# Kernel optimization log

Hardware: AMD Instinct MI355X
Metric: run time of the kernel (lower is better)

Reference implementation:

```python
import jax, jax.numpy as jnp
from jax import lax
import numpy as np

B, N, G, K = 4, 1024, 128, 32
D_MODEL, DEPTH, CLS = 384, 12, 40
D_INNER, D_STATE, D_CONV, DT_RANK = 768, 16, 4, 24
EPS = 1e-5
BN_SCALE = 1.0 / float(np.sqrt(1.0 + EPS))  # eval BN, running_mean=0, running_var=1


def layernorm(x, w, b):
    mu = x.mean(-1, keepdims=True)
    var = ((x - mu) ** 2).mean(-1, keepdims=True)
    return (x - mu) * lax.rsqrt(var + EPS) * w + b


def bn_eval(x, g, b):
    return x * (g * BN_SCALE) + b


def fps(xyz, n):
    Bb, Nn, _ = xyz.shape
    first = jnp.zeros((Bb,), jnp.int32)

    def step(carry, _):
        dmin, last = carry
        p = jnp.take_along_axis(xyz, last[:, None, None], axis=1)  # B,1,3
        dmin = jnp.minimum(dmin, jnp.sum((xyz - p) ** 2, -1))
        nxt = jnp.argmax(dmin, -1).astype(jnp.int32)
        return (dmin, nxt), nxt

    _, rest = lax.scan(step, (jnp.full((Bb, Nn), 1e10, xyz.dtype), first), None, length=n - 1)
    return jnp.concatenate([first[None, :], rest], 0).T  # B,G


def group_points(xyz):
    idx = fps(xyz, G)
    center = jnp.take_along_axis(xyz, idx[:, :, None], axis=1)            # B,G,3
    d2 = jnp.sum((center[:, :, None, :] - xyz[:, None, :, :]) ** 2, -1)   # B,G,N
    _, knn = lax.top_k(-d2, K)                                            # B,G,K
    nb = jax.vmap(lambda p, i: p[i])(xyz, knn)                            # B,G,K,3
    return nb - center[:, :, None, :], center


def encoder(pg, w1, b1, g1, bb1, w2, b2, w3, b3, g2, bb2, w4, b4):
    Bb, Gg, Kk, _ = pg.shape
    f = pg.reshape(Bb * Gg, Kk, 3)
    f = jax.nn.relu(bn_eval(f @ w1.T + b1, g1, bb1))                      # BG,K,128
    f = f @ w2.T + b2                                                     # BG,K,256
    fg = f.max(1, keepdims=True)
    f = jnp.concatenate([jnp.broadcast_to(fg, f.shape), f], -1)           # BG,K,512
    f = jax.nn.relu(bn_eval(f @ w3.T + b3, g2, bb2))
    f = f @ w4.T + b4
    return f.max(1).reshape(Bb, Gg, -1)                                   # B,G,C


def mamba_mixer(x, ipw, cw, cb, xpw, dpw, dpb, A_log, Dp, opw):
    L = x.shape[1]
    xz = x @ ipw.T                                                        # B,L,2*Di
    u, z = jnp.split(xz, 2, -1)
    up = jnp.pad(u, ((0, 0), (D_CONV - 1, 0), (0, 0)))                    # causal depthwise conv
    u = sum(up[:, k:k + L, :] * cw[:, k] for k in range(D_CONV)) + cb
    u = jax.nn.silu(u)
    xdb = u @ xpw.T
    dt, Bm, Cm = jnp.split(xdb, [DT_RANK, DT_RANK + D_STATE], -1)
    dt = jax.nn.softplus(dt @ dpw.T + dpb)                                # B,L,Di
    A = -jnp.exp(A_log)                                                   # Di,Ds

    def step(h, inp):
        dt_t, B_t, C_t, u_t = inp
        h = jnp.exp(dt_t[:, :, None] * A) * h + (dt_t * u_t)[:, :, None] * B_t[:, None, :]
        return h, jnp.einsum('bds,bs->bd', h, C_t)

    h0 = jnp.zeros((x.shape[0], D_INNER, D_STATE), x.dtype)
    _, ys = lax.scan(step, h0, (dt.swapaxes(0, 1), Bm.swapaxes(0, 1), Cm.swapaxes(0, 1), u.swapaxes(0, 1)))
    y = ys.swapaxes(0, 1) + u * Dp
    return (y * jax.nn.silu(z)) @ opw.T


def forward(pts, enc_w1, enc_b1, enc_bn1_g, enc_bn1_b, enc_w2, enc_b2, enc_w3, enc_b3,
            enc_bn2_g, enc_bn2_b, enc_w4, enc_b4, pos_w1, pos_b1, pos_w2, pos_b2,
            ln_w, ln_b, in_proj_w, conv_w, conv_b, x_proj_w, dt_proj_w, dt_proj_b,
            A_log, D_param, out_proj_w, normf_w, normf_b, norm_w, norm_b,
            head_w1, head_b1, head_bn1_g, head_bn1_b, head_w2, head_b2,
            head_bn2_g, head_bn2_b, head_w3, head_b3):
    nb, center = group_points(pts)
    tok = encoder(nb, enc_w1, enc_b1, enc_bn1_g, enc_bn1_b, enc_w2, enc_b2,
                  enc_w3, enc_b3, enc_bn2_g, enc_bn2_b, enc_w4, enc_b4)    # B,G,384
    pos = jax.nn.gelu(center @ pos_w1.T + pos_b1, approximate=False) @ pos_w2.T + pos_b2

    # PointMamba token reordering: sort by center x, y, z and concatenate -> L = 3G
    toks, poss = [], []
    for ax in range(3):
        o = jnp.argsort(center[:, :, ax], axis=-1)[:, :, None]
        toks.append(jnp.take_along_axis(tok, o, axis=1))
        poss.append(jnp.take_along_axis(pos, o, axis=1))
    tok = jnp.concatenate(toks, 1)
    pos = jnp.concatenate(poss, 1)

    h = tok + pos
    res = jnp.zeros_like(h)

    def layer_step(carry, p):
        h, res = carry
        lnw, lnb, ipw, cw, cb, xpw, dpw, dpb, Al, Dp, opw = p
        res = h + res
        x = layernorm(res, lnw, lnb)
        h = mamba_mixer(x, ipw, cw, cb, xpw, dpw, dpb, Al, Dp, opw)
        return (h, res), None

    (h, res), _ = lax.scan(layer_step, (h, res),
                           (ln_w, ln_b, in_proj_w, conv_w, conv_b, x_proj_w,
                            dt_proj_w, dt_proj_b, A_log, D_param, out_proj_w))
    x = layernorm(h + res, normf_w, normf_b)   # MixerModel.norm_f
    x = layernorm(x, norm_w, norm_b)           # PointMamba.norm
    feat = x.mean(1)                           # B,384
    h1 = jax.nn.relu(bn_eval(feat @ head_w1.T + head_b1, head_bn1_g, head_bn1_b))
    h2 = jax.nn.relu(bn_eval(h1 @ head_w2.T + head_b2, head_bn2_g, head_bn2_b))
    return h2 @ head_w3.T + head_b3            # B,CLS


def setup_inputs():
    key = jax.random.key(0)
    ks = iter(jax.random.split(key, 64))

    def rn(shape, s=0.02):
        return jax.random.normal(next(ks), shape, jnp.float32) * s

    inp = dict(
        pts=jax.random.normal(next(ks), (B, N, 3), jnp.float32),
        enc_w1=rn((128, 3), 0.1), enc_b1=jnp.zeros((128,)),
        enc_bn1_g=jnp.ones((128,)), enc_bn1_b=jnp.zeros((128,)),
        enc_w2=rn((256, 128), 0.05), enc_b2=jnp.zeros((256,)),
        enc_w3=rn((512, 512), 0.05), enc_b3=jnp.zeros((512,)),
        enc_bn2_g=jnp.ones((512,)), enc_bn2_b=jnp.zeros((512,)),
        enc_w4=rn((D_MODEL, 512), 0.05), enc_b4=jnp.zeros((D_MODEL,)),
        pos_w1=rn((128, 3), 0.1), pos_b1=jnp.zeros((128,)),
        pos_w2=rn((D_MODEL, 128), 0.05), pos_b2=jnp.zeros((D_MODEL,)),
        ln_w=jnp.ones((DEPTH, D_MODEL)), ln_b=jnp.zeros((DEPTH, D_MODEL)),
        in_proj_w=rn((DEPTH, 2 * D_INNER, D_MODEL)),
        conv_w=rn((DEPTH, D_INNER, D_CONV), 0.2), conv_b=jnp.zeros((DEPTH, D_INNER)),
        x_proj_w=rn((DEPTH, DT_RANK + 2 * D_STATE, D_INNER)),
        dt_proj_w=rn((DEPTH, D_INNER, DT_RANK), 0.1),
        dt_proj_b=jnp.full((DEPTH, D_INNER), -4.6, jnp.float32),
        A_log=jnp.broadcast_to(jnp.log(jnp.arange(1, D_STATE + 1, dtype=jnp.float32)),
                               (DEPTH, D_INNER, D_STATE)).copy(),
        D_param=jnp.ones((DEPTH, D_INNER)),
        out_proj_w=rn((DEPTH, D_MODEL, D_INNER)),
        normf_w=jnp.ones((D_MODEL,)), normf_b=jnp.zeros((D_MODEL,)),
        norm_w=jnp.ones((D_MODEL,)), norm_b=jnp.zeros((D_MODEL,)),
        head_w1=rn((256, D_MODEL), 0.05), head_b1=jnp.zeros((256,)),
        head_bn1_g=jnp.ones((256,)), head_bn1_b=jnp.zeros((256,)),
        head_w2=rn((256, 256), 0.05), head_b2=jnp.zeros((256,)),
        head_bn2_g=jnp.ones((256,)), head_bn2_b=jnp.zeros((256,)),
        head_w3=rn((CLS, 256), 0.05), head_b3=jnp.zeros((CLS,)),
    )
    return inp


def reference(pts, enc_w1, enc_b1, enc_bn1_g, enc_bn1_b, enc_w2, enc_b2, enc_w3, enc_b3,
              enc_bn2_g, enc_bn2_b, enc_w4, enc_b4, pos_w1, pos_b1, pos_w2, pos_b2,
              ln_w, ln_b, in_proj_w, conv_w, conv_b, x_proj_w, dt_proj_w, dt_proj_b,
              A_log, D_param, out_proj_w, normf_w, normf_b, norm_w, norm_b,
              head_w1, head_b1, head_bn1_g, head_bn1_b, head_w2, head_b2,
              head_bn2_g, head_bn2_b, head_w3, head_b3):
    return forward(pts, enc_w1, enc_b1, enc_bn1_g, enc_bn1_b, enc_w2, enc_b2, enc_w3, enc_b3,
                   enc_bn2_g, enc_bn2_b, enc_w4, enc_b4, pos_w1, pos_b1, pos_w2, pos_b2,
                   ln_w, ln_b, in_proj_w, conv_w, conv_b, x_proj_w, dt_proj_w, dt_proj_b,
                   A_log, D_param, out_proj_w, normf_w, normf_b, norm_w, norm_b,
                   head_w1, head_b1, head_bn1_g, head_bn1_b, head_w2, head_b2,
                   head_bn2_g, head_bn2_b, head_w3, head_b3)
```

## Files before the change

### kernel.cpp

```cpp
#include <hip/hip_runtime.h>
#include <hip/hip_bf16.h>

using bf16 = __hip_bfloat16;
using short8  = __attribute__((ext_vector_type(8))) short;
using floatx4 = __attribute__((ext_vector_type(4))) float;
using ull = unsigned long long;

constexpr int Bn = 4, Np = 1024, Gn = 128, Kn = 32;
constexpr int DM = 384, DEPTH = 12, CLSn = 40;
constexpr int DI = 768, DSt = 16, DTR = 24;
constexpr int Ln = 384;
constexpr int NCH = 12, CHS = 32;
constexpr int XDBS = 1536*56;
constexpr float EPSf = 1e-5f;
constexpr float BNS = 0.99999500003749968752f;
constexpr float LOG2E = 1.4426950408889634f;

static __device__ __forceinline__ short f2bf(float f){
  bf16 h = __float2bfloat16(f);
  return *reinterpret_cast<short*>(&h);
}
static __device__ __forceinline__ float fsig(float x){ return 1.f/(1.f + __expf(-x)); }
static __device__ __forceinline__ float fsoftplus(float x){
  return fmaxf(x, 0.f) + __logf(1.f + __expf(-fabsf(x)));
}

template<int CTRL>
static __device__ __forceinline__ int dppmov(int x){
  return __builtin_amdgcn_update_dpp(0, x, CTRL, 0xF, 0xF, true);
}
static __device__ __forceinline__ ull redmax64(ull key){
  #define RSTEP(CTRL) { \
    int hi = (int)(unsigned)(key >> 32), lo = (int)(unsigned)key; \
    int h2 = dppmov<CTRL>(hi), l2 = dppmov<CTRL>(lo); \
    ull k2 = ((ull)(unsigned)h2 << 32) | (unsigned)l2; \
    if (k2 > key) key = k2; }
  RSTEP(0x111) RSTEP(0x112) RSTEP(0x114) RSTEP(0x118) RSTEP(0x142) RSTEP(0x143)
  #undef RSTEP
  return key;
}

__global__ __launch_bounds__(256) void fps_kernel(const float* __restrict__ pts,
                                                  float* __restrict__ center){
  int b = blockIdx.x, t = threadIdx.x;
  int w = t >> 6, lane = t & 63;
  __shared__ float xs[1024], ys[1024], zs[1024];
  __shared__ ull red[2][4];
  const float* p = pts + (size_t)b * Np * 3;
  float X[4], Y[4], Z[4], D[4];
  #pragma unroll
  for (int i = 0; i < 4; ++i){
    int n = t + 256*i;
    float a = p[n*3+0], c = p[n*3+1], e = p[n*3+2];
    X[i] = a; Y[i] = c; Z[i] = e;
    xs[n] = a; ys[n] = c; zs[n] = e;
    D[i] = 1e10f;
  }
  __syncthreads();
  float px = xs[0], py = ys[0], pz = zs[0];
  if (t == 0){
    center[(size_t)(b*Gn)*3+0] = px;
    center[(size_t)(b*Gn)*3+1] = py;
    center[(size_t)(b*Gn)*3+2] = pz;
  }
  for (int it = 1; it < Gn; ++it){
    float v = -1.f; int nbest = t;
    #pragma unroll
    for (int i = 0; i < 4; ++i){
      float dx = __fsub_rn(X[i], px);
      float dy = __fsub_rn(Y[i], py);
      float dz = __fsub_rn(Z[i], pz);
      float d  = __fadd_rn(__fadd_rn(__fmul_rn(dx,dx), __fmul_rn(dy,dy)), __fmul_rn(dz,dz));
      float dm = fminf(D[i], d); D[i] = dm;
      if (dm > v){ v = dm; nbest = t + 256*i; }
    }
    ull key = ((ull)__float_as_uint(v) << 32) | (unsigned)(Np-1 - nbest);
    key = redmax64(key);
    if (lane == 63) red[it & 1][w] = key;
    __syncthreads();
    ull k = red[it & 1][0];
    #pragma unroll
    for (int j = 1; j < 4; ++j){ ull kj = red[it & 1][j]; if (kj > k) k = kj; }
    int wn = Np-1 - (int)(unsigned)(k & 0xFFFFFFFFu);
    wn = min(max(wn, 0), Np-1);
    px = xs[wn]; py = ys[wn]; pz = zs[wn];
    if (t == 0){
      center[(size_t)(b*Gn+it)*3+0] = px;
      center[(size_t)(b*Gn+it)*3+1] = py;
      center[(size_t)(b*Gn+it)*3+2] = pz;
    }
  }
}

__global__ __launch_bounds__(256) void knn_kernel(const float* __restrict__ pts,
                                                  const float* __restrict__ center,
                                                  float* __restrict__ nb){
  int gid = blockIdx.x; int b = gid >> 7;
  __shared__ float d2[1024];
  __shared__ float rv[4]; __shared__ int ri[4];
  int t = threadIdx.x;
  float cx = center[(size_t)gid*3+0], cy = center[(size_t)gid*3+1], cz = center[(size_t)gid*3+2];
  const float* p = pts + (size_t)b * Np * 3;
  for (int n = t; n < Np; n += 256){
    float dx = __fsub_rn(cx, p[n*3+0]);
    float dy = __fsub_rn(cy, p[n*3+1]);
    float dz = __fsub_rn(cz, p[n*3+2]);
    d2[n] = __fadd_rn(__fadd_rn(__fmul_rn(dx,dx), __fmul_rn(dy,dy)), __fmul_rn(dz,dz));
  }
  __syncthreads();
  for (int kk = 0; kk < Kn; ++kk){
    float v = 3e38f; int idx = 0;
    for (int n = t; n < Np; n += 256){
      float d = d2[n];
      if (d < v || (d == v && n < idx)){ v = d; idx = n; }
    }
    ull key = ((ull)(unsigned)(~__float_as_uint(v)) << 32) | (unsigned)(Np-1 - idx);
    key = redmax64(key);
    if ((t & 63) == 63){
      rv[t>>6] = __uint_as_float(~(unsigned)(key >> 32));
      ri[t>>6] = Np-1 - (int)(unsigned)(key & 0xFFFFFFFFu);
    }
    __syncthreads();
    if (t == 0){
      float bv = rv[0]; int bi = ri[0];
      for (int w = 1; w < 4; ++w){
        if (rv[w] < bv || (rv[w] == bv && ri[w] < bi)){ bv = rv[w]; bi = ri[w]; }
      }
      bi = min(max(bi, 0), Np-1);
      nb[((size_t)gid*Kn+kk)*3+0] = __fsub_rn(p[bi*3+0], cx);
      nb[((size_t)gid*Kn+kk)*3+1] = __fsub_rn(p[bi*3+1], cy);
      nb[((size_t)gid*Kn+kk)*3+2] = __fsub_rn(p[bi*3+2], cz);
      d2[bi] = 3e38f;
    }
    __syncthreads();
  }
}

__global__ __launch_bounds__(256) void cvt_all(const float* __restrict__ s0,
    const float* __restrict__ s1, const float* __restrict__ s2,
    const float* __restrict__ s3, const float* __restrict__ s4,
    const float* __restrict__ s5, bf16* __restrict__ dst){
  long i = ((long)blockIdx.x*256 + threadIdx.x)*4;
  if (i >= 11624448L) return;
  const float* s; long off;
  if      (i <  7077888L){ s = s0; off = 0L; }
  else if (i < 10616832L){ s = s1; off =  7077888L; }
  else if (i < 11132928L){ s = s2; off = 10616832L; }
  else if (i < 11165696L){ s = s3; off = 11132928L; }
  else if (i < 11427840L){ s = s4; off = 11165696L; }
  else                   { s = s5; off = 11427840L; }
  float4 v = *(const float4*)(s + (i - off));
  short* o = (short*)dst + i;
  o[0] = f2bf(v.x); o[1] = f2bf(v.y); o[2] = f2bf(v.z); o[3] = f2bf(v.w);
}

template<typename AT, typename WT, int ACT, int MODE, typename CT = float>
__global__ __launch_bounds__(256) void gemm_mfma(const AT* __restrict__ A, int lda,
                                                 const WT* __restrict__ W,
                                                 const float* __restrict__ bias,
                                                 const float* __restrict__ gz,
                                                 const float* __restrict__ bbp,
                                                 CT* __restrict__ C, int ldc,
                                                 int M, int N, int K){
  __shared__ __align__(16) short As[64*40];
  __shared__ __align__(16) short Ws[64*40];
  int bm = blockIdx.x * 64, bn = blockIdx.y * 64;
  int t = threadIdx.x;
  int row = t >> 2;
  int kseg = (t & 3) * 8;
  int w = t >> 6, lane = t & 63, m16 = lane & 15, q = lane >> 4;
  floatx4 acc[4] = {};
  for (int k0 = 0; k0 < K; k0 += 32){
    {
      const float* Ar = (const float*)A + (size_t)(bm + row)*lda;
      short* dst = &As[row*40 + kseg];
      #pragma unroll
      for (int j = 0; j < 8; ++j){
        int k = k0 + kseg + j;
        dst[j] = (k < K) ? f2bf(Ar[k]) : (short)0;
      }
    }
    {
      int n = bn + row;
      short* dst = &Ws[row*40 + kseg];
      #pragma unroll
      for (int j = 0; j < 8; ++j){
        int k = k0 + kseg + j;
        dst[j] = (n < N && k < K) ? f2bf(((const float*)W)[(size_t)n*K + k]) : (short)0;
      }
    }
    __syncthreads();
    short8 af = *(const short8*)&As[(w*16 + m16)*40 + q*8];
    #pragma unroll
    for (int j = 0; j < 4; ++j){
      short8 bfr = *(const short8*)&Ws[(j*16 + m16)*40 + q*8];
      acc[j] = __builtin_amdgcn_mfma_f32_16x16x32_bf16(af, bfr, acc[j], 0, 0, 0);
    }
    __syncthreads();
  }
  #pragma unroll
  for (int j = 0; j < 4; ++j){
    int n = bn + j*16 + m16;
    if (n < N){
      float bv = bias ? bias[n] : 0.f;
      float gv = 0.f, bbv = 0.f;
      if (ACT == 1){ gv = gz[n] * BNS; bbv = bbp[n]; }
      #pragma unroll
      for (int r = 0; r < 4; ++r){
        int m = bm + w*16 + q*4 + r;
        float v = acc[j][r] + bv;
        if (ACT == 1){ v = v * gv + bbv; v = fmaxf(v, 0.f); }
        if constexpr (sizeof(CT) == 2) C[(size_t)m*ldc + n] = __float2bfloat16(v);
        else                           C[(size_t)m*ldc + n] = v;
      }
    }
  }
}

template<typename AT, typename WT, int ACT, int MODE, typename CT = float>
__global__ __launch_bounds__(256) void gemm_mfma64(const AT* __restrict__ A, int lda,
                                                   const WT* __restrict__ W,
                                                   const float* __restrict__ bias,
                                                   const float* __restrict__ gz,
                                                   const float* __restrict__ bbp,
                                                   CT* __restrict__ C, int ldc,
                                                   int M, int N, int K){
  __shared__ __align__(16) short As[64*72];
  __shared__ __align__(16) short Ws[64*72];
  int bm = blockIdx.x * 64, bn = blockIdx.y * 64;
  int t = threadIdx.x;
  int row = t >> 2;
  int kseg = (t & 3) * 16;
  int w = t >> 6, lane = t & 63, m16 = lane & 15, q = lane >> 4;
  floatx4 acc[4] = {};
  for (int k0 = 0; k0 < K; k0 += 64){
    if constexpr (MODE == 1){
      const float* Yr = (const float*)A + (size_t)(bm + row)*lda + k0 + kseg;
      const float* Zr = gz + (size_t)(bm + row)*1536 + 768 + k0 + kseg;
      float y[16], z[16];
      #pragma unroll
      for (int j = 0; j < 4; ++j){
        *(float4*)&y[j*4] = *(const float4*)(Yr + j*4);
        *(float4*)&z[j*4] = *(const float4*)(Zr + j*4);
      }
      short* dst = &As[row*72 + kseg];
      #pragma unroll
      for (int jj = 0; jj < 16; ++jj) dst[jj] = f2bf(y[jj] * (z[jj] * fsig(z[jj])));
    } else if constexpr (sizeof(AT) == 2){
      const short* Ar = (const short*)A + (size_t)(bm + row)*lda + k0 + kseg;
      *(short8*)&As[row*72 + kseg]     = *(const short8*)Ar;
      *(short8*)&As[row*72 + kseg + 8] = *(const short8*)(Ar + 8);
    } else {
      const float* Ar = (const float*)A + (size_t)(bm + row)*lda + k0 + kseg;
      float a[16];
      #pragma unroll
      for (int j = 0; j < 4; ++j) *(float4*)&a[j*4] = *(const float4*)(Ar + j*4);
      short* dst = &As[row*72 + kseg];
      #pragma unroll
      for (int jj = 0; jj < 16; ++jj) dst[jj] = f2bf(a[jj]);
    }
    {
      int n = bn + row;
      if constexpr (sizeof(WT) == 2){
        short8 v0, v1;
        #pragma unroll
        for (int j = 0; j < 8; ++j){ v0[j] = 0; v1[j] = 0; }
        if (n < N){
          const short* Wr = (const short*)W + (size_t)n*K + k0 + kseg;
          v0 = *(const short8*)Wr;
          v1 = *(const short8*)(Wr + 8);
        }
        *(short8*)&Ws[row*72 + kseg]     = v0;
        *(short8*)&Ws[row*72 + kseg + 8] = v1;
      } else {
        short* dst = &Ws[row*72 + kseg];
        if (n < N){
          const float* Wr = (const float*)W + (size_t)n*K + k0 + kseg;
          float wv[16];
          #pragma unroll
          for (int j = 0; j < 4; ++j) *(float4*)&wv[j*4] = *(const float4*)(Wr + j*4);
          #pragma unroll
          for (int jj = 0; jj < 16; ++jj) dst[jj] = f2bf(wv[jj]);
        } else {
          #pragma unroll
          for (int jj = 0; jj < 16; ++jj) dst[jj] = 0;
        }
      }
    }
    __syncthreads();
    short8 af0 = *(const short8*)&As[(w*16 + m16)*72 + q*8];
    short8 af1 = *(const short8*)&As[(w*16 + m16)*72 + 32 + q*8];
    #pragma unroll
    for (int j = 0; j < 4; ++j){
      short8 b0 = *(const short8*)&Ws[(j*16 + m16)*72 + q*8];
      acc[j] = __builtin_amdgcn_mfma_f32_16x16x32_bf16(af0, b0, acc[j], 0, 0, 0);
      short8 b1 = *(const short8*)&Ws[(j*16 + m16)*72 + 32 + q*8];
      acc[j] = __builtin_amdgcn_mfma_f32_16x16x32_bf16(af1, b1, acc[j], 0, 0, 0);
    }
    __syncthreads();
  }
  #pragma unroll
  for (int j = 0; j < 4; ++j){
    int n = bn + j*16 + m16;
    if (n < N){
      float bv = bias ? bias[n] : 0.f;
      float gv = 0.f, bbv = 0.f;
      if (ACT == 1){ gv = gz[n] * BNS; bbv = bbp[n]; }
      #pragma unroll
      for (int r = 0; r < 4; ++r){
        int m = bm + w*16 + q*4 + r;
        float v = acc[j][r] + bv;
        if (ACT == 1){ v = v * gv + bbv; v = fmaxf(v, 0.f); }
        if constexpr (sizeof(CT) == 2) C[(size_t)m*ldc + n] = __float2bfloat16(v);
        else                           C[(size_t)m*ldc + n] = v;
      }
    }
  }
}

template<typename AT, typename WT, int ACT, typename CT = float>
__global__ __launch_bounds__(256) void gemm_mfma128(const AT* __restrict__ A, int lda,
                                                    const WT* __restrict__ W,
                                                    const float* __restrict__ bias,
                                                    const float* __restrict__ gz,
                                                    const float* __restrict__ bbp,
                                                    CT* __restrict__ C, int ldc,
                                                    int M, int N, int K){
  __shared__ __align__(16) short As[64*72];
  __shared__ __align__(16) short Ws[128*72];
  int bm = blockIdx.x * 64, bn = blockIdx.y * 128;
  int t = threadIdx.x;
  int row = t >> 2;
  int kseg = (t & 3) * 16;
  int row2 = t >> 1;
  int kseg2 = (t & 1) * 32;
  int w = t >> 6, lane = t & 63, m16 = lane & 15, q = lane >> 4;
  floatx4 acc[8] = {};
  for (int k0 = 0; k0 < K; k0 += 64){
    if constexpr (sizeof(AT) == 2){
      const short* Ar = (const short*)A + (size_t)(bm + row)*lda + k0 + kseg;
      *(short8*)&As[row*72 + kseg]     = *(const short8*)Ar;
      *(short8*)&As[row*72 + kseg + 8] = *(const short8*)(Ar + 8);
    } else {
      const float* Ar = (const float*)A + (size_t)(bm + row)*lda + k0 + kseg;
      float a[16];
      #pragma unroll
      for (int j = 0; j < 4; ++j) *(float4*)&a[j*4] = *(const float4*)(Ar + j*4);
      short* dst = &As[row*72 + kseg];
      #pragma unroll
      for (int jj = 0; jj < 16; ++jj) dst[jj] = f2bf(a[jj]);
    }
    {
      int n = bn + row2;
      if constexpr (sizeof(WT) == 2){
        short8 v0, v1, v2, v3;
        #pragma unroll
        for (int j = 0; j < 8; ++j){ v0[j] = 0; v1[j] = 0; v2[j] = 0; v3[j] = 0; }
        if (n < N){
          const short* Wr = (const short*)W + (size_t)n*K + k0 + kseg2;
          v0 = *(const short8*)Wr;
          v1 = *(const short8*)(Wr + 8);
          v2 = *(const short8*)(Wr + 16);
          v3 = *(const short8*)(Wr + 24);
        }
        *(short8*)&Ws[row2*72 + kseg2]      = v0;
        *(short8*)&Ws[row2*72 + kseg2 + 8]  = v1;
        *(short8*)&Ws[row2*72 + kseg2 + 16] = v2;
        *(short8*)&Ws[row2*72 + kseg2 + 24] = v3;
      } else {
        short* dst = &Ws[row2*72 + kseg2];
        if (n < N){
          const float* Wr = (const float*)W + (size_t)n*K + k0 + kseg2;
          float wv[32];
          #pragma unroll
          for (int j = 0; j < 8; ++j) *(float4*)&wv[j*4] = *(const float4*)(Wr + j*4);
          #pragma unroll
          for (int jj = 0; jj < 32; ++jj) dst[jj] = f2bf(wv[jj]);
        } else {
          #pragma unroll
          for (int jj = 0; jj < 32; ++jj) dst[jj] = 0;
        }
      }
    }
    __syncthreads();
    short8 af0 = *(const short8*)&As[(w*16 + m16)*72 + q*8];
    short8 af1 = *(const short8*)&As[(w*16 + m16)*72 + 32 + q*8];
    #pragma unroll
    for (int j = 0; j < 8; ++j){
      short8 b0 = *(const short8*)&Ws[(j*16 + m16)*72 + q*8];
      acc[j] = __builtin_amdgcn_mfma_f32_16x16x32_bf16(af0, b0, acc[j], 0, 0, 0);
      short8 b1 = *(const short8*)&Ws[(j*16 + m16)*72 + 32 + q*8];
      acc[j] = __builtin_amdgcn_mfma_f32_16x16x32_bf16(af1, b1, acc[j], 0, 0, 0);
    }
    __syncthreads();
  }
  #pragma unroll
  for (int j = 0; j < 8; ++j){
    int n = bn + j*16 + m16;
    if (n < N){
      float bv = bias ? bias[n] : 0.f;
      float gv = 0.f, bbv = 0.f;
      if (ACT == 1){ gv = gz[n] * BNS; bbv = bbp[n]; }
      #pragma unroll
      for (int r = 0; r < 4; ++r){
        int m = bm + w*16 + q*4 + r;
        float v = acc[j][r] + bv;
        if (ACT == 1){ v = v * gv + bbv; v = fmaxf(v, 0.f); }
        if constexpr (sizeof(CT) == 2) C[(size_t)m*ldc + n] = __float2bfloat16(v);
        else                           C[(size_t)m*ldc + n] = v;
      }
    }
  }
}

template<typename WT>
__global__ __launch_bounds__(256) void xproj_kernel(const float* __restrict__ xz,
                                                    const WT* __restrict__ W,
                                                    const float* __restrict__ cw,
                                                    const float* __restrict__ cb,
                                                    float* __restrict__ xdbp,
                                                    int KB){
  __shared__ __align__(16) short As[64*72];
  __shared__ __align__(16) short Ws[64*72];
  int bm = blockIdx.x * 64;
  int ks = blockIdx.y;
  int t = threadIdx.x;
  int row = t >> 2, kseg = (t & 3) * 16;
  int w = t >> 6, lane = t & 63, m16 = lane & 15, q = lane >> 4;
  int m = bm + row;
  int l = m % Ln;
  const int kbase = ks * KB;
  floatx4 acc[4] = {};
  const float4 z4 = make_float4(0.f, 0.f, 0.f, 0.f);
  for (int k0 = kbase; k0 < kbase + KB; k0 += 64){
    {
      int ch = k0 + kseg;
      const float* base = xz + (size_t)m*1536 + ch;
      float x0[16], x1[16], x2[16], x3[16];
      #pragma unroll
      for (int j4 = 0; j4 < 4; ++j4){
        *(float4*)&x3[j4*4] = *(const float4*)(base + j4*4);
        *(float4*)&x2[j4*4] = (l >= 1) ? *(const float4*)(base - 1536 + j4*4) : z4;
        *(float4*)&x1[j4*4] = (l >= 2) ? *(const float4*)(base - 2*1536 + j4*4) : z4;
        *(float4*)&x0[j4*4] = (l >= 3) ? *(const float4*)(base - 3*1536 + j4*4) : z4;
      }
      short* dst = &As[row*72 + kseg];
      #pragma unroll
      for (int j = 0; j < 16; ++j){
        float4 wv = *(const float4*)(cw + (size_t)(ch + j)*4);
        float v = x0[j]*wv.x + x1[j]*wv.y + x2[j]*wv.z + x3[j]*wv.w + cb[ch + j];
        v = v * fsig(v);
        dst[j] = f2bf(v);
      }
    }
    {
      int n = row;
      if constexpr (sizeof(WT) == 2){
        short8 v0, v1;
        #pragma unroll
        for (int j = 0; j < 8; ++j){ v0[j] = 0; v1[j] = 0; }
        if (n < 56){
          const short* Wr = (const short*)W + (size_t)n*DI + k0 + kseg;
          v0 = *(const short8*)Wr;
          v1 = *(const short8*)(Wr + 8);
        }
        *(short8*)&Ws[row*72 + kseg]     = v0;
        *(short8*)&Ws[row*72 + kseg + 8] = v1;
      } else {
        short* dst = &Ws[row*72 + kseg];
        if (n < 56){
          const float* Wr = (const float*)W + (size_t)n*DI + k0 + kseg;
          float wv[16];
          #pragma unroll
          for (int j = 0; j < 4; ++j) *(float4*)&wv[j*4] = *(const float4*)(Wr + j*4);
          #pragma unroll
          for (int jj = 0; jj < 16; ++jj) dst[jj] = f2bf(wv[jj]);
        } else {
          #pragma unroll
          for (int jj = 0; jj < 16; ++jj) dst[jj] = 0;
        }
      }
    }
    __syncthreads();
    short8 af0 = *(const short8*)&As[(w*16 + m16)*72 + q*8];
    short8 af1 = *(const short8*)&As[(w*16 + m16)*72 + 32 + q*8];
    #pragma unroll
    for (int j = 0; j < 4; ++j){
      short8 b0 = *(const short8*)&Ws[(j*16 + m16)*72 + q*8];
      acc[j] = __builtin_amdgcn_mfma_f32_16x16x32_bf16(af0, b0, acc[j], 0, 0, 0);
      short8 b1 = *(const short8*)&Ws[(j*16 + m16)*72 + 32 + q*8];
      acc[j] = __builtin_amdgcn_mfma_f32_16x16x32_bf16(af1, b1, acc[j], 0, 0, 0);
    }
    __syncthreads();
  }
  float* C = xdbp + (size_t)ks * XDBS;
  #pragma unroll
  for (int j = 0; j < 4; ++j){
    int n = j*16 + m16;
    if (n < 56){
      #pragma unroll
      for (int r = 0; r < 4; ++r){
        int mm = bm + w*16 + q*4 + r;
        C[(size_t)mm*56 + n] = acc[j][r];
      }
    }
  }
}

__global__ __launch_bounds__(256) void maxk_fg(float* __restrict__ f3in){
  int gg = blockIdx.x; int c = threadIdx.x;
  float m = -3e38f;
  for (int k = 0; k < Kn; ++k) m = fmaxf(m, f3in[((size_t)gg*Kn + k)*512 + 256 + c]);
  for (int k = 0; k < Kn; ++k) f3in[((size_t)gg*Kn + k)*512 + c] = m;
}

__global__ __launch_bounds__(256) void maxk_fg_bf(bf16* __restrict__ f3b){
  int gg = blockIdx.x; int c = threadIdx.x;
  float m = -3e38f;
  for (int k = 0; k < Kn; ++k) m = fmaxf(m, __bfloat162float(f3b[((size_t)gg*Kn + k)*512 + 256 + c]));
  bf16 mv = __float2bfloat16(m);
  for (int k = 0; k < Kn; ++k) f3b[((size_t)gg*Kn + k)*512 + c] = mv;
}

__global__ __launch_bounds__(384) void maxk_tok(const float* __restrict__ f4, float* __restrict__ tok){
  int gg = blockIdx.x; int c = threadIdx.x;
  float m = -3e38f;
  for (int k = 0; k < Kn; ++k) m = fmaxf(m, f4[((size_t)gg*Kn + k)*DM + c]);
  tok[(size_t)gg*DM + c] = m;
}

__global__ __launch_bounds__(128) void pos_kernel(const float* __restrict__ center,
                                                  const float* __restrict__ w1, const float* __restrict__ b1,
                                                  const float* __restrict__ w2, const float* __restrict__ b2,
                                                  float* __restrict__ tok){
  int gid = blockIdx.x;
  __shared__ float h1[128]; __shared__ float c3[3];
  int t = threadIdx.x;
  if (t < 3) c3[t] = center[(size_t)gid*3 + t];
  __syncthreads();
  float a = w1[t*3+0]*c3[0] + w1[t*3+1]*c3[1] + w1[t*3+2]*c3[2] + b1[t];
  h1[t] = 0.5f * a * (1.f + erff(a * 0.70710678118654752440f));
  __syncthreads();
  for (int c = t; c < DM; c += 128){
    float s = b2[c];
    for (int j = 0; j < 128; ++j) s += w2[(size_t)c*128 + j] * h1[j];
    tok[(size_t)gid*DM + c] += s;
  }
}

__global__ __launch_bounds__(128) void sort_kernel(const float* __restrict__ center,
                                                   int* __restrict__ order){
  int bax = blockIdx.x; int b = bax / 3, ax = bax % 3;
  __shared__ float key[128];
  int t = threadIdx.x;
  key[t] = center[(size_t)(b*Gn + t)*3 + ax];
  __syncthreads();
  float kt = key[t]; int r = 0;
  for (int j = 0; j < Gn; ++j){
    float kj = key[j];
    r += (kj < kt || (kj == kt && j < t)) ? 1 : 0;
  }
  r = min(max(r, 0), Gn-1);
  order[b*Ln + ax*Gn + r] = t;
}

__global__ __launch_bounds__(256) void build_h(const float* __restrict__ tok,
                        const int* __restrict__ order,
                        float* __restrict__ h, float* __restrict__ res){
  int i = blockIdx.x * blockDim.x + threadIdx.x;
  if (i >= Bn*Ln*DM) return;
  int c = i % DM; int l = (i / DM) % Ln; int b = i / (DM*Ln);
  int src = order[b*Ln + l];
  src = min(max(src, 0), Gn-1);
  h[i] = tok[((size_t)(b*Gn + src))*DM + c];
  res[i] = 0.f;
}

__global__ __launch_bounds__(256) void ln_res_kernel(const float* __restrict__ h,
                                                     float* __restrict__ res,
                                                     bf16* __restrict__ x,
                                                     const float* __restrict__ w,
                                                     const float* __restrict__ bias){
  int wv = threadIdx.x >> 6, ln = threadIdx.x & 63;
  int tokid = blockIdx.x*4 + wv;
  const float* hr = h + (size_t)tokid*DM;
  float* rr = res + (size_t)tokid*DM;
  bf16* xr = x + (size_t)tokid*DM;
  float v[6]; float s = 0.f;
  #pragma unroll
  for (int i = 0; i < 6; ++i){ int c = ln + 64*i; float t = hr[c] + rr[c]; rr[c] = t; v[i] = t; s += t; }
  #pragma unroll
  for (int o = 32; o > 0; o >>= 1) s += __shfl_xor(s, o);
  float mu = s * (1.f/DM);
  float q = 0.f;
  #pragma unroll
  for (int i = 0; i < 6; ++i){ float d = v[i] - mu; q += d*d; }
  #pragma unroll
  for (int o = 32; o > 0; o >>= 1) q += __shfl_xor(q, o);
  float rstd = rsqrtf(q * (1.f/DM) + EPSf);
  #pragma unroll
  for (int i = 0; i < 6; ++i){ int c = ln + 64*i;
    xr[c] = __float2bfloat16((v[i]-mu)*rstd*w[c] + bias[c]); }
}

__global__ __launch_bounds__(256) void scanA_kernel(const float* __restrict__ xz,
                                                    const float* __restrict__ xdbp, int nks,
                                                    const float* __restrict__ cw,
                                                    const float* __restrict__ cb,
                                                    const float* __restrict__ dpw,
                                                    const float* __restrict__ dpb,
                                                    const float* __restrict__ A_log,
                                                    float* __restrict__ SB_S,
                                                    float* __restrict__ SB_dt,
                                                    float* __restrict__ BND){
  __shared__ float sRow[CHS*56];
  __shared__ float sU[CHS*256];
  int blk = blockIdx.x;
  int c = blk % NCH; int bd = blk / NCH; int dch = bd % 3; int b = bd / 3;
  int t = threadIdx.x; int d = dch*256 + t;
  int l0 = c*CHS;
  for (int i = t; i < CHS*56; i += 256){
    size_t base = ((size_t)(b*Ln + l0))*56 + i;
    float s = xdbp[base];
    for (int k = 1; k < nks; ++k) s += xdbp[(size_t)k*XDBS + base];
    sRow[i] = s;
  }
  float xv[CHS+3];
  #pragma unroll
  for (int j = 0; j < 3; ++j){
    int ll = l0 - 3 + j;
    xv[j] = (ll >= 0) ? xz[((size_t)(b*Ln + ll))*1536 + d] : 0.f;
  }
  const float* xp = xz + ((size_t)(b*Ln + l0))*1536 + d;
  #pragma unroll
  for (int i = 0; i < CHS; ++i) xv[3+i] = xp[(size_t)i*1536];
  #pragma unroll
  for (int j = 0; j < 3; ++j) BND[((size_t)blk*3 + j)*256 + t] = xv[j];
  float cw0 = cw[d*4+0], cw1 = cw[d*4+1], cw2 = cw[d*4+2], cw3 = cw[d*4+3];
  float cbv = cb[d];
  #pragma unroll
  for (int i = 0; i < CHS; ++i){
    float v = xv[i]*cw0 + xv[i+1]*cw1 + xv[i+2]*cw2 + xv[i+3]*cw3 + cbv;
    sU[i*256 + t] = v * fsig(v);
  }
  float w[DTR];
  const float* wp = dpw + (size_t)d*DTR;
  #pragma unroll
  for (int j = 0; j < DTR; ++j) w[j] = wp[j];
  float a2[DSt], h[DSt];
  const float* ap = A_log + (size_t)d*DSt;
  #pragma unroll
  for (int s = 0; s < DSt; ++s){ a2[s] = -__expf(ap[s]) * LOG2E; h[s] = 0.f; }
  float dbias = dpb[d];
  float sumdt = 0.f;
  __syncthreads();
  for (int i = 0; i < CHS; ++i){
    int ro = i*56;
    float dtr = dbias;
    #pragma unroll
    for (int j = 0; j < DTR; ++j) dtr += w[j] * sRow[ro + j];
    float dtv = fsoftplus(dtr);
    sumdt += dtv;
    float du = dtv * sU[i*256 + t];
    #pragma unroll
    for (int s = 0; s < DSt; ++s)
      h[s] = exp2f(dtv * a2[s]) * h[s] + du * sRow[ro + 24 + s];
  }
  size_t sb = ((size_t)blk*256 + t)*16;
  #pragma unroll
  for (int s = 0; s < DSt; ++s) SB_S[sb + s] = h[s];
  SB_dt[(size_t)blk*256 + t] = sumdt;
}

__global__ __launch_bounds__(256) void scanB_kernel(float* __restrict__ xz,
                                                    const float* __restrict__ xdbp, int nks,
                                                    const float* __restrict__ cw,
                                                    const float* __restrict__ cb,
                                                    const float* __restrict__ dpw,
                                                    const float* __restrict__ dpb,
                                                    const float* __restrict__ A_log,
                                                    const float* __restrict__ Dp,
                                                    const float* __restrict__ SB_S,
                                                    const float* __restrict__ SB_dt,
                                                    const float* __restrict__ BND,
                                                    bf16* __restrict__ yb){
  __shared__ float sRow[CHS*56];
  __shared__ float sU[CHS*256];
  int blk = blockIdx.x;
  int c = blk % NCH; int bd = blk / NCH; int dch = bd % 3; int b = bd / 3;
  int t = threadIdx.x; int d = dch*256 + t;
  int l0 = c*CHS;
  for (int i = t; i < CHS*56; i += 256){
    size_t base = ((size_t)(b*Ln + l0))*56 + i;
    float s = xdbp[base];
    for (int k = 1; k < nks; ++k) s += xdbp[(size_t)k*XDBS + base];
    sRow[i] = s;
  }
  float xv[CHS+3];
  #pragma unroll
  for (int j = 0; j < 3; ++j) xv[j] = BND[((size_t)blk*3 + j)*256 + t];
  const float* xp = xz + ((size_t)(b*Ln + l0))*1536 + d;
  #pragma unroll
  for (int i = 0; i < CHS; ++i) xv[3+i] = xp[(size_t)i*1536];
  float cw0 = cw[d*4+0], cw1 = cw[d*4+1], cw2 = cw[d*4+2], cw3 = cw[d*4+3];
  float cbv = cb[d];
  #pragma unroll
  for (int i = 0; i < CHS; ++i){
    float v = xv[i]*cw0 + xv[i+1]*cw1 + xv[i+2]*cw2 + xv[i+3]*cw3 + cbv;
    sU[i*256 + t] = v * fsig(v);
  }
  float w[DTR];
  const float* wp = dpw + (size_t)d*DTR;
  #pragma unroll
  for (int j = 0; j < DTR; ++j) w[j] = wp[j];
  float a2[DSt], h[DSt];
  const float* ap = A_log + (size_t)d*DSt;
  #pragma unroll
  for (int s = 0; s < DSt; ++s){ a2[s] = -__expf(ap[s]) * LOG2E; h[s] = 0.f; }
  for (int cc = 0; cc < c; ++cc){
    size_t base = (((size_t)bd*NCH + cc)*256 + t)*16;
    float sd = SB_dt[((size_t)bd*NCH + cc)*256 + t];
    #pragma unroll
    for (int s = 0; s < DSt; ++s)
      h[s] = exp2f(sd * a2[s]) * h[s] + SB_S[base + s];
  }
  float dbias = dpb[d];
  float Dd = Dp[d];
  float* ydst = xz + ((size_t)(b*Ln + l0))*1536 + dch*256;
  const float* zrow = xz + ((size_t)(b*Ln + l0))*1536 + 768 + dch*256;
  bf16* ybr = yb ? (yb + ((size_t)(b*Ln + l0))*DI + dch*256) : nullptr;
  __syncthreads();
  for (int i = 0; i < CHS; ++i){
    int ro = i*56;
    float dtr = dbias;
    #pragma unroll
    for (int j = 0; j < DTR; ++j) dtr += w[j] * sRow[ro + j];
    float dtv = fsoftplus(dtr);
    float u = sU[i*256 + t];
    float du = dtv * u;
    float yv = 0.f;
    #pragma unroll
    for (int s = 0; s < DSt; ++s){
      h[s] = exp2f(dtv * a2[s]) * h[s] + du * sRow[ro + 24 + s];
      yv += h[s] * sRow[ro + 40 + s];
    }
    float yfull = yv + u*Dd;
    if (ybr){
      float zv = zrow[(size_t)i*1536 + t];
      ybr[(size_t)i*DI + t] = __float2bfloat16(yfull * (zv * fsig(zv)));
    } else {
      ydst[(size_t)i*1536 + t] = yfull;
    }
  }
}

__global__ __launch_bounds__(256) void final_ln_kernel(const float* __restrict__ h,
                                                       const float* __restrict__ res,
                                                       const float* w1, const float* b1,
                                                       const float* w2, const float* b2,
                                                       float* __restrict__ x){
  int wv = threadIdx.x >> 6, ln = threadIdx.x & 63;
  int tokid = blockIdx.x*4 + wv;
  const float* hr = h + (size_t)tokid*DM;
  const float* rr = res + (size_t)tokid*DM;
  float* xr = x + (size_t)tokid*DM;
  float v[6]; float s = 0.f;
  #pragma unroll
  for (int i = 0; i < 6; ++i){ int c = ln + 64*i; v[i] = hr[c] + rr[c]; s += v[i]; }
  #pragma unroll
  for (int o = 32; o > 0; o >>= 1) s += __shfl_xor(s, o);
  float mu = s * (1.f/DM); float q = 0.f;
  #pragma unroll
  for (int i = 0; i < 6; ++i){ float dd = v[i]-mu; q += dd*dd; }
  #pragma unroll
  for (int o = 32; o > 0; o >>= 1) q += __shfl_xor(q, o);
  float rstd = rsqrtf(q * (1.f/DM) + EPSf);
  float u[6]; float s2 = 0.f;
  #pragma unroll
  for (int i = 0; i < 6; ++i){ int c = ln + 64*i; u[i] = (v[i]-mu)*rstd*w1[c] + b1[c]; s2 += u[i]; }
  #pragma unroll
  for (int o = 32; o > 0; o >>= 1) s2 += __shfl_xor(s2, o);
  float mu2 = s2 * (1.f/DM); float q2 = 0.f;
  #pragma unroll
  for (int i = 0; i < 6; ++i){ float dd = u[i]-mu2; q2 += dd*dd; }
  #pragma unroll
  for (int o = 32; o > 0; o >>= 1) q2 += __shfl_xor(q2, o);
  float rstd2 = rsqrtf(q2 * (1.f/DM) + EPSf);
  #pragma unroll
  for (int i = 0; i < 6; ++i){ int c = ln + 64*i; xr[c] = (u[i]-mu2)*rstd2*w2[c] + b2[c]; }
}

__global__ __launch_bounds__(384) void mean_kernel(const float* __restrict__ x,
                                                   float* __restrict__ featp){
  int blk = blockIdx.x;
  int b = blk >> 2, g = blk & 3;
  int c = threadIdx.x;
  const float* xp = x + ((size_t)(b*Ln + g*96))*DM + c;
  float a0=0.f,a1=0.f,a2=0.f,a3=0.f,a4=0.f,a5=0.f,a6=0.f,a7=0.f;
  for (int l = 0; l < 96; l += 8){
    a0 += xp[(size_t)(l+0)*DM];
    a1 += xp[(size_t)(l+1)*DM];
    a2 += xp[(size_t)(l+2)*DM];
    a3 += xp[(size_t)(l+3)*DM];
    a4 += xp[(size_t)(l+4)*DM];
    a5 += xp[(size_t)(l+5)*DM];
    a6 += xp[(size_t)(l+6)*DM];
    a7 += xp[(size_t)(l+7)*DM];
  }
  featp[(size_t)blk*DM + c] = ((a0+a1)+(a2+a3)) + ((a4+a5)+(a6+a7));
}

__global__ __launch_bounds__(256) void head_mlp(const float* __restrict__ featp,
    const float* w1, const float* b1, const float* g1, const float* bb1,
    const float* w2, const float* b2, const float* g2, const float* bb2,
    const float* w3, const float* b3, float* __restrict__ out){
  int b = blockIdx.x; int t = threadIdx.x;
  __shared__ float f[DM]; __shared__ float h1[256]; __shared__ float h2[256];
  for (int i = t; i < DM; i += 256){
    f[i] = (featp[(size_t)(b*4+0)*DM + i] + featp[(size_t)(b*4+1)*DM + i]
          + featp[(size_t)(b*4+2)*DM + i] + featp[(size_t)(b*4+3)*DM + i]) * (1.f/Ln);
  }
  __syncthreads();
  {
    float a = b1[t];
    #pragma unroll 4
    for (int j = 0; j < DM; ++j) a += w1[(size_t)t*DM + j] * f[j];
    a = a * (g1[t] * BNS) + bb1[t];
    h1[t] = fmaxf(a, 0.f);
  }
  __syncthreads();
  {
    float a = b2[t];
    #pragma unroll 4
    for (int j = 0; j < 256; ++j) a += w2[(size_t)t*256 + j] * h1[j];
    a = a * (g2[t] * BNS) + bb2[t];
    h2[t] = fmaxf(a, 0.f);
  }
  __syncthreads();
  if (t < CLSn){
    float a = b3[t];
    for (int j = 0; j < 256; ++j) a += w3[(size_t)t*256 + j] * h2[j];
    out[b*CLSn + t] = a;
  }
}

extern "C" void kernel_launch(void* const* d_in, const int* in_sizes, int n_in,
                              void* d_out, int out_size, void* d_ws, size_t ws_size,
                              hipStream_t stream) {
  if (n_in < 42) return;
  if (out_size < Bn*CLSn) return;
  constexpr size_t WS_FLOATS = 3919936;
  if (ws_size < WS_FLOATS * sizeof(float)) return;
  constexpr size_t MIDF = 5812224;
  constexpr size_t BIGF = 18874368;
  const bool mid = ws_size >= (WS_FLOATS + MIDF) * sizeof(float);
  const bool big = ws_size >= (WS_FLOATS + MIDF + BIGF) * sizeof(float);

  const float* pts       = (const float*)d_in[0];
  const float* enc_w1    = (const float*)d_in[1];  const float* enc_b1    = (const float*)d_in[2];
  const float* enc_bn1_g = (const float*)d_in[3];  const float* enc_bn1_b = (const float*)d_in[4];
  const float* enc_w2    = (const float*)d_in[5];  const float* enc_b2    = (const float*)d_in[6];
  const float* enc_w3    = (const float*)d_in[7];  const float* enc_b3    = (const float*)d_in[8];
  const float* enc_bn2_g = (const float*)d_in[9];  const float* enc_bn2_b = (const float*)d_in[10];
  const float* enc_w4    = (const float*)d_in[11]; const float* enc_b4    = (const float*)d_in[12];
  const float* pos_w1    = (const float*)d_in[13]; const float* pos_b1    = (const float*)d_in[14];
  const float* pos_w2    = (const float*)d_in[15]; const float* pos_b2    = (const float*)d_in[16];
  const float* ln_w      = (const float*)d_in[17]; const float* ln_b      = (const float*)d_in[18];
  const float* in_proj_w = (const float*)d_in[19];
  const float* conv_w    = (const float*)d_in[20]; const float* conv_b    = (const float*)d_in[21];
  const float* x_proj_w  = (const float*)d_in[22];
  const float* dt_proj_w = (const float*)d_in[23]; const float* dt_proj_b = (const float*)d_in[24];
  const float* A_log     = (const float*)d_in[25]; const float* D_param   = (const float*)d_in[26];
  const float* out_proj_w= (const float*)d_in[27];
  const float* normf_w   = (const float*)d_in[28]; const float* normf_b   = (const float*)d_in[29];
  const float* norm_w    = (const float*)d_in[30]; const float* norm_b    = (const float*)d_in[31];
  const float* head_w1   = (const float*)d_in[32]; const float* head_b1   = (const float*)d_in[33];
  const float* head_bn1_g= (const float*)d_in[34]; const float* head_bn1_b= (const float*)d_in[35];
  const float* head_w2   = (const float*)d_in[36]; const float* head_b2   = (const float*)d_in[37];
  const float* head_bn2_g= (const float*)d_in[38]; const float* head_bn2_b= (const float*)d_in[39];
  const float* head_w3   = (const float*)d_in[40]; const float* head_b3   = (const float*)d_in[41];

  float* ws = (float*)d_ws;
  float* hb   = ws;
  float* resb = ws + 589824;
  float* U    = ws + 1179648;
  float* center = U;
  float* nb     = U + 1536;
  float* tok    = U + 50688;
  int*   order  = (int*)(U + 247296);
  float* eb0    = U + 262144;
  float* eb1    = U + 1310720;
  float* xz   = U;
  float* xdb  = U + 2359296;
  bf16*  xb   = (bf16*)(U + 2445312);
  float* SBdt_s = U + 2445312;
  float* BND  = U + 2482176;
  float* SBS_s  = hb;
  float* xf   = U;
  float* featp = U + 589824;
  float* WB = ws + WS_FLOATS;
  bf16* wb_ip = (bf16*)WB;
  bf16* wb_op = (bf16*)(WB + 3538944);
  bf16* wb_xp = (bf16*)(WB + 5308416);
  bf16* wb_e2 = (bf16*)(WB + 5566464);
  bf16* wb_e3 = (bf16*)(WB + 5582848);
  bf16* wb_e4 = (bf16*)(WB + 5713920);
  float* BIGB = WB + MIDF;
  bf16*  F1b  = (bf16*)BIGB;
  bf16*  F3b  = (bf16*)(BIGB + 1048576);
  bf16*  F3c  = (bf16*)(BIGB + 5242880);
  float* F4   = BIGB + 9437184;
  float* xdbp_b = BIGB + 15728640;
  float* SBS_b  = BIGB + 16072704;
  float* SBdt_b = BIGB + 16662528;
  bf16*  yb     = (bf16*)(BIGB + 16699392);

  if (mid)
    cvt_all<<<11352, 256, 0, stream>>>(in_proj_w, out_proj_w, x_proj_w,
                                       enc_w2, enc_w3, enc_w4, (bf16*)WB);

  fps_kernel<<<Bn, 256, 0, stream>>>(pts, center);
  knn_kernel<<<Bn*Gn, 256, 0, stream>>>(pts, center, nb);

  if (big){
    gemm_mfma<float,float,1,0,bf16><<<dim3(256,2), 256, 0, stream>>>(nb, 3, enc_w1, enc_b1,
        enc_bn1_g, enc_bn1_b, F1b, 128, 16384, 128, 3);
    gemm_mfma128<bf16,bf16,0,bf16><<<dim3(256,2), 256, 0, stream>>>(F1b, 128, wb_e2, enc_b2,
        nullptr, nullptr, F3b + 256, 512, 16384, 256, 128);
    maxk_fg_bf<<<512, 256, 0, stream>>>(F3b);
    gemm_mfma128<bf16,bf16,1,bf16><<<dim3(256,4), 256, 0, stream>>>(F3b, 512, wb_e3, enc_b3,
        enc_bn2_g, enc_bn2_b, F3c, 512, 16384, 512, 512);
    gemm_mfma128<bf16,bf16,0,float><<<dim3(256,3), 256, 0, stream>>>(F3c, 512, wb_e4, enc_b4,
        nullptr, nullptr, F4, 384, 16384, 384, 512);
    maxk_tok<<<512, 384, 0, stream>>>(F4, tok);
  } else {
    for (int ch = 0; ch < 8; ++ch){
      const float* nb_c = nb + (size_t)ch*2048*3;
      float* tok_c = tok + (size_t)ch*64*DM;
      gemm_mfma<float,float,1,0><<<dim3(32,2), 256, 0, stream>>>(nb_c, 3, enc_w1, enc_b1,
          enc_bn1_g, enc_bn1_b, eb1, 128, 2048, 128, 3);
      if (mid){
        gemm_mfma64<float,bf16,0,0><<<dim3(32,4), 256, 0, stream>>>(eb1, 128, wb_e2, enc_b2,
            nullptr, nullptr, eb0 + 256, 512, 2048, 256, 128);
        maxk_fg<<<64, 256, 0, stream>>>(eb0);
        gemm_mfma64<float,bf16,1,0><<<dim3(32,8), 256, 0, stream>>>(eb0, 512, wb_e3, enc_b3,
            enc_bn2_g, enc_bn2_b, eb1, 512, 2048, 512, 512);
        gemm_mfma64<float,bf16,0,0><<<dim3(32,6), 256, 0, stream>>>(eb1, 512, wb_e4, enc_b4,
            nullptr, nullptr, eb0, 384, 2048, 384, 512);
      } else {
        gemm_mfma64<float,float,0,0><<<dim3(32,4), 256, 0, stream>>>(eb1, 128, enc_w2, enc_b2,
            nullptr, nullptr, eb0 + 256, 512, 2048, 256, 128);
        maxk_fg<<<64, 256, 0, stream>>>(eb0);
        gemm_mfma64<float,float,1,0><<<dim3(32,8), 256, 0, stream>>>(eb0, 512, enc_w3, enc_b3,
            enc_bn2_g, enc_bn2_b, eb1, 512, 2048, 512, 512);
        gemm_mfma64<float,float,0,0><<<dim3(32,6), 256, 0, stream>>>(eb1, 512, enc_w4, enc_b4,
            nullptr, nullptr, eb0, 384, 2048, 384, 512);
      }
      maxk_tok<<<64, 384, 0, stream>>>(eb0, tok_c);
    }
  }

  pos_kernel<<<Bn*Gn, 128, 0, stream>>>(center, pos_w1, pos_b1, pos_w2, pos_b2, tok);
  sort_kernel<<<Bn*3, 128, 0, stream>>>(center, order);
  build_h<<<(Bn*Ln*DM + 255)/256, 256, 0, stream>>>(tok, order, hb, resb);

  const int nks = big ? 4 : 1;
  float* xdbp = big ? xdbp_b : xdb;
  float* SBS  = big ? SBS_b  : SBS_s;
  float* SBdt = big ? SBdt_b : SBdt_s;

  for (int l = 0; l < DEPTH; ++l){
    const float* lnw  = ln_w      + (size_t)l*DM;
    const float* lnb  = ln_b      + (size_t)l*DM;
    const float* ipw  = in_proj_w + (size_t)l*1536*DM;
    const float* cw   = conv_w    + (size_t)l*DI*4;
    const float* cb   = conv_b    + (size_t)l*DI;
    const float* xpw  = x_proj_w  + (size_t)l*56*DI;
    const float* dpw  = dt_proj_w + (size_t)l*DI*DTR;
    const float* dpb  = dt_proj_b + (size_t)l*DI;
    const float* Alg  = A_log     + (size_t)l*DI*DSt;
    const float* Dpar = D_param   + (size_t)l*DI;
    const float* opw  = out_proj_w+ (size_t)l*DM*DI;

    ln_res_kernel<<<Bn*Ln/4, 256, 0, stream>>>(hb, resb, xb, lnw, lnb);
    if (mid){
      gemm_mfma128<bf16,bf16,0,float><<<dim3(24,12), 256, 0, stream>>>(xb, DM,
          wb_ip + (size_t)l*1536*DM, nullptr, nullptr, nullptr, xz, 1536, Bn*Ln, 1536, DM);
    } else {
      gemm_mfma128<bf16,float,0,float><<<dim3(24,12), 256, 0, stream>>>(xb, DM, ipw,
          nullptr, nullptr, nullptr, xz, 1536, Bn*Ln, 1536, DM);
    }
    if (mid)
      xproj_kernel<bf16><<<dim3(24, nks), 256, 0, stream>>>(xz,
          wb_xp + (size_t)l*56*DI, cw, cb, xdbp, DI/nks);
    else
      xproj_kernel<float><<<dim3(24, nks), 256, 0, stream>>>(xz,
          xpw, cw, cb, xdbp, DI/nks);
    scanA_kernel<<<Bn*3*NCH, 256, 0, stream>>>(xz, xdbp, nks, cw, cb,
        dpw, dpb, Alg, SBS, SBdt, BND);
    scanB_kernel<<<Bn*3*NCH, 256, 0, stream>>>(xz, xdbp, nks, cw, cb,
        dpw, dpb, Alg, Dpar, SBS, SBdt, BND, big ? yb : nullptr);
    if (big){
      gemm_mfma64<bf16,bf16,0,0><<<dim3(24,6), 256, 0, stream>>>(yb, DI,
          wb_op + (size_t)l*DM*DI, nullptr, nullptr, nullptr, hb, DM, Bn*Ln, DM, DI);
    } else if (mid){
      gemm_mfma64<float,bf16,0,1><<<dim3(24,6), 256, 0, stream>>>(xz, 1536,
          wb_op + (size_t)l*DM*DI, nullptr, xz, nullptr, hb, DM, Bn*Ln, DM, DI);
    } else {
      gemm_mfma64<float,float,0,1><<<dim3(24,6), 256, 0, stream>>>(xz, 1536, opw,
          nullptr, xz, nullptr, hb, DM, Bn*Ln, DM, DI);
    }
  }

  final_ln_kernel<<<Bn*Ln/4, 256, 0, stream>>>(hb, resb, normf_w, normf_b, norm_w, norm_b, xf);
  mean_kernel<<<Bn*4, 384, 0, stream>>>(xf, featp);
  head_mlp<<<Bn, 256, 0, stream>>>(featp, head_w1, head_b1, head_bn1_g, head_bn1_b,
                                   head_w2, head_b2, head_bn2_g, head_bn2_b,
                                   head_w3, head_b3, (float*)d_out);
}
```

Measured before the change: 1.812 ms.

## Fuse per-group max pooling into encoder GEMM epilogues and drop pooling kernels

Adds a POOL template mode to the 128-wide MFMA GEMM. Mode 1 computes the per-group column max in the epilogue and broadcasts it into the concat half of the buffer, replacing maxk_fg_bf. Mode 2 writes only the pooled token row, removing the F4 intermediate buffer and the maxk_tok kernel. This cuts large intermediate writes and reads and two launches, and shrinks the big workspace requirement. The FPS kernel also stores points as float4 in shared memory so the chosen center is fetched with one load, and uses a tree max for the final wave reduction.

Result: no change. 1.801 ms (-0.6%).

```diff
diff --git a/kernel.cpp b/kernel.cpp
--- a/kernel.cpp
+++ b/kernel.cpp
@@ -24,6 +24,7 @@
 static __device__ __forceinline__ float fsoftplus(float x){
   return fmaxf(x, 0.f) + __logf(1.f + __expf(-fabsf(x)));
 }
+static __device__ __forceinline__ ull umax64(ull a, ull b){ return a > b ? a : b; }
 
 template<int CTRL>
 static __device__ __forceinline__ int dppmov(int x){
@@ -44,7 +45,7 @@
                                                   float* __restrict__ center){
   int b = blockIdx.x, t = threadIdx.x;
   int w = t >> 6, lane = t & 63;
-  __shared__ float xs[1024], ys[1024], zs[1024];
+  __shared__ float4 P[1024];
   __shared__ ull red[2][4];
   const float* p = pts + (size_t)b * Np * 3;
   float X[4], Y[4], Z[4], D[4];
@@ -53,11 +54,12 @@
     int n = t + 256*i;
     float a = p[n*3+0], c = p[n*3+1], e = p[n*3+2];
     X[i] = a; Y[i] = c; Z[i] = e;
-    xs[n] = a; ys[n] = c; zs[n] = e;
+    P[n] = make_float4(a, c, e, 0.f);
     D[i] = 1e10f;
   }
   __syncthreads();
-  float px = xs[0], py = ys[0], pz = zs[0];
+  float4 c0 = P[0];
+  float px = c0.x, py = c0.y, pz = c0.z;
   if (t == 0){
     center[(size_t)(b*Gn)*3+0] = px;
     center[(size_t)(b*Gn)*3+1] = py;
@@ -78,12 +80,12 @@
     key = redmax64(key);
     if (lane == 63) red[it & 1][w] = key;
     __syncthreads();
-    ull k = red[it & 1][0];
-    #pragma unroll
-    for (int j = 1; j < 4; ++j){ ull kj = red[it & 1][j]; if (kj > k) k = kj; }
+    ull k = umax64(umax64(red[it & 1][0], red[it & 1][1]),
+                   umax64(red[it & 1][2], red[it & 1][3]));
     int wn = Np-1 - (int)(unsigned)(k & 0xFFFFFFFFu);
     wn = min(max(wn, 0), Np-1);
-    px = xs[wn]; py = ys[wn]; pz = zs[wn];
+    float4 cc = P[wn];
+    px = cc.x; py = cc.y; pz = cc.z;
     if (t == 0){
       center[(size_t)(b*Gn+it)*3+0] = px;
       center[(size_t)(b*Gn+it)*3+1] = py;
@@ -318,7 +320,7 @@
   }
 }
 
-template<typename AT, typename WT, int ACT, typename CT = float>
+template<typename AT, typename WT, int ACT, typename CT, int POOL>
 __global__ __launch_bounds__(256) void gemm_mfma128(const AT* __restrict__ A, int lda,
                                                     const WT* __restrict__ W,
                                                     const float* __restrict__ bias,
@@ -394,21 +396,64 @@
     }
     __syncthreads();
   }
+  float val[8][4];
   #pragma unroll
   for (int j = 0; j < 8; ++j){
     int n = bn + j*16 + m16;
-    if (n < N){
-      float bv = bias ? bias[n] : 0.f;
-      float gv = 0.f, bbv = 0.f;
-      if (ACT == 1){ gv = gz[n] * BNS; bbv = bbp[n]; }
-      #pragma unroll
-      for (int r = 0; r < 4; ++r){
-        int m = bm + w*16 + q*4 + r;
-        float v = acc[j][r] + bv;
-        if (ACT == 1){ v = v * gv + bbv; v = fmaxf(v, 0.f); }
-        if constexpr (sizeof(CT) == 2) C[(size_t)m*ldc + n] = __float2bfloat16(v);
-        else                           C[(size_t)m*ldc + n] = v;
-      }
+    float bv = (bias && n < N) ? bias[n] : 0.f;
+    float gv = 0.f, bbv = 0.f;
+    if (ACT == 1 && n < N){ gv = gz[n] * BNS; bbv = bbp[n]; }
+    #pragma unroll
+    for (int r = 0; r < 4; ++r){
+      float v = acc[j][r] + bv;
+      if (ACT == 1){ v = v * gv + bbv; v = fmaxf(v, 0.f); }
+      val[j][r] = v;
+    }
+  }
+  if constexpr (POOL == 0){
+    #pragma unroll
+    for (int j = 0; j < 8; ++j){
+      int n = bn + j*16 + m16;
+      if (n < N){
+        #pragma unroll
+        for (int r = 0; r < 4; ++r){
+          int m = bm + w*16 + q*4 + r;
+          if constexpr (sizeof(CT) == 2) C[(size_t)m*ldc + n] = __float2bfloat16(val[j][r]);
+          else                           C[(size_t)m*ldc + n] = val[j][r];
+        }
+      }
+    }
+  } else {
+    float* mat = (float*)As;
+    #pragma unroll
+    for (int j = 0; j < 8; ++j){
+      float lm = fmaxf(fmaxf(val[j][0], val[j][1]), fmaxf(val[j][2], val[j][3]));
+      mat[(w*4 + q)*128 + j*16 + m16] = lm;
+    }
+    if constexpr (POOL == 1){
+      #pragma unroll
+      for (int j = 0; j < 8; ++j){
+        int n = bn + j*16 + m16;
+        #pragma unroll
+        for (int r = 0; r < 4; ++r){
+          int m = bm + w*16 + q*4 + r;
+          C[(size_t)m*ldc + n] = __float2bfloat16(val[j][r]);
+        }
+      }
+    }
+    __syncthreads();
+    int col = t & 127, half = t >> 7;
+    float gm = mat[(half*8)*128 + col];
+    #pragma unroll
+    for (int s = 1; s < 8; ++s) gm = fmaxf(gm, mat[(half*8 + s)*128 + col]);
+    if constexpr (POOL == 1){
+      bf16 gb = __float2bfloat16(gm);
+      bf16* dst = (bf16*)C - 256 + (size_t)(bm + half*32)*ldc + bn + col;
+      #pragma unroll
+      for (int rr = 0; rr < 32; ++rr) dst[(size_t)rr*ldc] = gb;
+    } else {
+      int g = (bm >> 5) + half;
+      ((float*)C)[(size_t)g*ldc + bn + col] = gm;
     }
   }
 }
@@ -514,14 +559,6 @@
   for (int k = 0; k < Kn; ++k) f3in[((size_t)gg*Kn + k)*512 + c] = m;
 }
 
-__global__ __launch_bounds__(256) void maxk_fg_bf(bf16* __restrict__ f3b){
-  int gg = blockIdx.x; int c = threadIdx.x;
-  float m = -3e38f;
-  for (int k = 0; k < Kn; ++k) m = fmaxf(m, __bfloat162float(f3b[((size_t)gg*Kn + k)*512 + 256 + c]));
-  bf16 mv = __float2bfloat16(m);
-  for (int k = 0; k < Kn; ++k) f3b[((size_t)gg*Kn + k)*512 + c] = mv;
-}
-
 __global__ __launch_bounds__(384) void maxk_tok(const float* __restrict__ f4, float* __restrict__ tok){
   int gg = blockIdx.x; int c = threadIdx.x;
   float m = -3e38f;
@@ -852,7 +889,7 @@
   constexpr size_t WS_FLOATS = 3919936;
   if (ws_size < WS_FLOATS * sizeof(float)) return;
   constexpr size_t MIDF = 5812224;
-  constexpr size_t BIGF = 18874368;
+  constexpr size_t BIGF = 9437184;
   const bool mid = ws_size >= (WS_FLOATS + MIDF) * sizeof(float);
   const bool big = ws_size >= (WS_FLOATS + MIDF + BIGF) * sizeof(float);
 
@@ -909,11 +946,10 @@
   bf16*  F1b  = (bf16*)BIGB;
   bf16*  F3b  = (bf16*)(BIGB + 1048576);
   bf16*  F3c  = (bf16*)(BIGB + 5242880);
-  float* F4   = BIGB + 9437184;
-  float* xdbp_b = BIGB + 15728640;
-  float* SBS_b  = BIGB + 16072704;
-  float* SBdt_b = BIGB + 16662528;
-  bf16*  yb     = (bf16*)(BIGB + 16699392);
+  float* xdbp_b = BIGB;
+  float* SBS_b  = BIGB + 344064;
+  float* SBdt_b = BIGB + 933888;
+  bf16*  yb     = (bf16*)(BIGB + 970752);
 
   if (mid)
     cvt_all<<<11352, 256, 0, stream>>>(in_proj_w, out_proj_w, x_proj_w,
@@ -925,14 +961,12 @@
   if (big){
     gemm_mfma<float,float,1,0,bf16><<<dim3(256,2), 256, 0, stream>>>(nb, 3, enc_w1, enc_b1,
         enc_bn1_g, enc_bn1_b, F1b, 128, 16384, 128, 3);
-    gemm_mfma128<bf16,bf16,0,bf16><<<dim3(256,2), 256, 0, stream>>>(F1b, 128, wb_e2, enc_b2,
+    gemm_mfma128<bf16,bf16,0,bf16,1><<<dim3(256,2), 256, 0, stream>>>(F1b, 128, wb_e2, enc_b2,
         nullptr, nullptr, F3b + 256, 512, 16384, 256, 128);
-    maxk_fg_bf<<<512, 256, 0, stream>>>(F3b);
-    gemm_mfma128<bf16,bf16,1,bf16><<<dim3(256,4), 256, 0, stream>>>(F3b, 512, wb_e3, enc_b3,
+    gemm_mfma128<bf16,bf16,1,bf16,0><<<dim3(256,4), 256, 0, stream>>>(F3b, 512, wb_e3, enc_b3,
         enc_bn2_g, enc_bn2_b, F3c, 512, 16384, 512, 512);
-    gemm_mfma128<bf16,bf16,0,float><<<dim3(256,3), 256, 0, stream>>>(F3c, 512, wb_e4, enc_b4,
-        nullptr, nullptr, F4, 384, 16384, 384, 512);
-    maxk_tok<<<512, 384, 0, stream>>>(F4, tok);
+    gemm_mfma128<bf16,bf16,0,float,2><<<dim3(256,3), 256, 0, stream>>>(F3c, 512, wb_e4, enc_b4,
+        nullptr, nullptr, tok, DM, 16384, 384, 512);
   } else {
     for (int ch = 0; ch < 8; ++ch){
       const float* nb_c = nb + (size_t)ch*2048*3;
@@ -984,10 +1018,10 @@
 
     ln_res_kernel<<<Bn*Ln/4, 256, 0, stream>>>(hb, resb, xb, lnw, lnb);
     if (mid){
-      gemm_mfma128<bf16,bf16,0,float><<<dim3(24,12), 256, 0, stream>>>(xb, DM,
+      gemm_mfma128<bf16,bf16,0,float,0><<<dim3(24,12), 256, 0, stream>>>(xb, DM,
           wb_ip + (size_t)l*1536*DM, nullptr, nullptr, nullptr, xz, 1536, Bn*Ln, 1536, DM);
     } else {
-      gemm_mfma128<bf16,float,0,float><<<dim3(24,12), 256, 0, stream>>>(xb, DM, ipw,
+      gemm_mfma128<bf16,float,0,float,0><<<dim3(24,12), 256, 0, stream>>>(xb, DM, ipw,
           nullptr, nullptr, nullptr, xz, 1536, Bn*Ln, 1536, DM);
     }
     if (mid)
```
